# Performance work log

Hardware: AMD Instinct MI355X
Metric: run time of the kernel (lower is better)

## Reference

```python
import jax, jax.numpy as jnp
import numpy as np

NH = 8
DIM = 512
NP = 1024
MNP = 4096
BS = 4
TOPK = 32


def setup_inputs() -> dict:
    key = jax.random.key(0)
    ks = jax.random.split(key, 10)
    q = jax.random.normal(ks[0], (NP, BS, DIM), dtype=jnp.float32)
    k = jax.random.normal(ks[1], (MNP, BS, DIM), dtype=jnp.float32)
    v = jax.random.normal(ks[2], (MNP, BS, DIM), dtype=jnp.float32)
    rns_indices = jax.random.randint(ks[3], (BS, NP, TOPK), 0, MNP)
    s = 0.02
    W1 = jax.random.normal(ks[4], (DIM, DIM), dtype=jnp.float32) * s
    b1 = jnp.zeros((DIM,), dtype=jnp.float32)
    W2 = jax.random.normal(ks[5], (DIM, DIM), dtype=jnp.float32) * s
    b2 = jnp.zeros((DIM,), dtype=jnp.float32)
    W3 = jax.random.normal(ks[6], (DIM, DIM), dtype=jnp.float32) * s
    b3 = jnp.zeros((DIM,), dtype=jnp.float32)
    return {"q": q, "k": k, "v": v, "rns_indices": rns_indices,
            "W1": W1, "b1": b1, "W2": W2, "b2": b2, "W3": W3, "b3": b3}


def reference(q, k, v, rns_indices, W1, b1, W2, b2, W3, b3):
    np_, bs, dim = q.shape
    mnp = k.shape[0]
    nh = NH
    dh = dim // nh
    # seq-first -> batch-first, linear projections (torch Linear: x @ W.T + b)
    qh = (jnp.einsum('nbd,ed->bne', q, W1) + b1).reshape(bs, np_, nh, dh)
    kh = (jnp.einsum('mbd,ed->bme', k, W2) + b2).reshape(bs, mnp, nh, dh)
    vh = (jnp.einsum('mbd,ed->bme', v, W3) + b3).reshape(bs, mnp, nh, dh)
    # dense scores: [bs, nh, np, mnp]
    w = jnp.einsum('bnhd,bmhd->bhnm', qh, kh) / jnp.sqrt(jnp.asarray(dh, w_dtype := qh.dtype))
    # scatter-built neighbor mask: [bs, np, mnp] (shared across heads)
    b_idx = jnp.arange(bs)[:, None, None]
    n_idx = jnp.arange(np_)[None, :, None]
    mask = jnp.zeros((bs, np_, mnp), dtype=w.dtype).at[b_idx, n_idx, rns_indices].set(1.0)
    mask = mask[:, None, :, :]  # broadcast over heads
    w = w * mask + (-1e9) * (1.0 - mask)
    w = jax.nn.softmax(w, axis=3)
    out = jnp.einsum('bhnm,bmhd->nbhd', w, vh).reshape(np_, bs, dim)
    return out
```

## Files before the change

kernel.cpp:

```cpp
#include <hip/hip_runtime.h>
#include <stdint.h>

#define NH   8
#define DIM  512
#define NP   1024
#define MNP  4096
#define BS   4
#define TOPK 32
#define DH   64

typedef unsigned short u16;
typedef __attribute__((ext_vector_type(8))) short bf16x8;
typedef __attribute__((ext_vector_type(4))) float f32x4;

__device__ __forceinline__ u16 f2bf(float f) {
    union { float f; unsigned u; } x; x.f = f;
    unsigned r = x.u + 0x7FFFu + ((x.u >> 16) & 1u);
    return (u16)(r >> 16);
}
__device__ __forceinline__ float bf2f(u16 h) {
    union { unsigned u; float f; } x; x.u = ((unsigned)h) << 16;
    return x.f;
}

__device__ __forceinline__ void async16(const void* g, void* l) {
    __builtin_amdgcn_global_load_lds(
        (const __attribute__((address_space(1))) unsigned int*)g,
        (__attribute__((address_space(3))) unsigned int*)l, 16, 0, 0);
}

__global__ void cvt_all(const float* __restrict__ W1, const float* __restrict__ W2,
                        const float* __restrict__ W3, const float* __restrict__ q,
                        const float* __restrict__ k,  const float* __restrict__ v,
                        u16* __restrict__ wall, u16* __restrict__ act) {
    size_t i = ((size_t)blockIdx.x * 256 + threadIdx.x) * 4;
    const float* s; u16* d;
    if (i < 786432) {
        d = wall + i;
        s = (i < 262144) ? W1 + i : (i < 524288) ? W2 + (i - 262144) : W3 + (i - 524288);
    } else {
        size_t j = i - 786432;
        d = act + j;
        s = (j < 2097152) ? q + j : (j < 10485760) ? k + (j - 2097152) : v + (j - 10485760);
    }
    float4 val = *(const float4*)s;
    ushort4 o;
    o.x = f2bf(val.x); o.y = f2bf(val.y); o.z = f2bf(val.z); o.w = f2bf(val.w);
    *(ushort4*)d = o;
}

__global__ __launch_bounds__(256, 2)
void proj_gemm(const u16* __restrict__ act, const u16* __restrict__ wall,
               const float* __restrict__ b1, const float* __restrict__ b2,
               const float* __restrict__ b3, u16* __restrict__ outall) {
    __shared__ u16 As[128 * 64];
    __shared__ u16 Bs[128 * 64];

    const int z = blockIdx.z;
    if (z == 0 && blockIdx.y >= 32) return;
    const size_t aoff = (z == 0) ? 0u : (z == 1) ? 2097152u : 10485760u;
    const u16* A = act + aoff;
    const u16* W = wall + (size_t)z * 262144;
    const float* bias = (z == 0) ? b1 : (z == 1) ? b2 : b3;
    u16* C = outall + aoff;

    const int tid  = threadIdx.x;
    const int bm   = blockIdx.y * 128;
    const int bn   = blockIdx.x * 128;
    const int wave = tid >> 6;
    const int lane = tid & 63;
    const int wm   = (wave & 1) * 64;
    const int wn   = (wave >> 1) * 64;
    const int l16  = lane & 15;
    const int quad = lane >> 4;

    const int srow = lane >> 3;
    const int scol = (lane & 7) * 8;

    f32x4 acc[4][4] = {};

    for (int k0 = 0; k0 < 512; k0 += 64) {
        __syncthreads();
#pragma unroll
        for (int r = 0; r < 4; r++) {
            int row = wave * 32 + r * 8;
            async16(A + (size_t)(bm + row + srow) * 512 + k0 + scol,
                    &As[row * 64 + lane * 8]);
            async16(W + (size_t)(bn + row + srow) * 512 + k0 + scol,
                    &Bs[row * 64 + lane * 8]);
        }
        __syncthreads();
#pragma unroll
        for (int kk = 0; kk < 64; kk += 32) {
            bf16x8 af[4], bfr[4];
#pragma unroll
            for (int i = 0; i < 4; i++) {
                af[i]  = *(const bf16x8*)(&As[(wm + i * 16 + l16) * 64 + kk + quad * 8]);
                bfr[i] = *(const bf16x8*)(&Bs[(wn + i * 16 + l16) * 64 + kk + quad * 8]);
            }
#pragma unroll
            for (int i = 0; i < 4; i++)
#pragma unroll
                for (int j = 0; j < 4; j++)
                    acc[i][j] = __builtin_amdgcn_mfma_f32_16x16x32_bf16(
                        af[i], bfr[j], acc[i][j], 0, 0, 0);
        }
    }
#pragma unroll
    for (int i = 0; i < 4; i++) {
        int row = bm + wm + i * 16 + quad * 4;
#pragma unroll
        for (int j = 0; j < 4; j++) {
            int col = bn + wn + j * 16 + l16;
            float bv = bias[col];
#pragma unroll
            for (int r = 0; r < 4; r++)
                C[(size_t)(row + r) * 512 + col] = f2bf(acc[i][j][r] + bv);
        }
    }
}

__global__ __launch_bounds__(256)
void attn_kernel(const u16* __restrict__ Qh, const u16* __restrict__ Kh,
                 const u16* __restrict__ Vh, const int* __restrict__ rns,
                 float* __restrict__ out) {
    __shared__ float sq[NH * 72];
    __shared__ int   sidx[TOPK];
    __shared__ int   srow[TOPK];
    __shared__ float sval[TOPK];
    __shared__ float ss[TOPK][9];
    __shared__ float sw[TOPK][9];

    const int bid = blockIdx.x;
    const int n = bid >> 2;
    const int b = bid & 3;
    const int tid = threadIdx.x;
    const int lane = tid & 63;

    if (tid < TOPK) {
        int mi = rns[((b * NP + n) * TOPK) + tid];
        sidx[tid] = mi;
        srow[tid] = (mi * BS + b) * DIM;
    }
    {
        const u16* qrow = Qh + (size_t)(n * BS + b) * DIM;
        unsigned int u = *(const unsigned int*)(qrow + tid * 2);
        int e0 = tid * 2;
        sq[(e0 >> 6) * 72 + (e0 & 63)]       = bf2f((u16)(u & 0xffff));
        sq[(e0 >> 6) * 72 + ((e0 + 1) & 63)] = bf2f((u16)(u >> 16));
    }
    __syncthreads();
    if (tid < TOPK) {
        float v = 1.0f;
        int me = sidx[tid];
        for (int j = 0; j < tid; j++)
            if (sidx[j] == me) v = 0.0f;
        sval[tid] = v;
    }
    __syncthreads();
    {
        const int i = tid >> 3;
        const int h = tid & 7;
        const u16* krow = Kh + srow[i] + h * DH;
        const float* qh = sq + h * 72;
        float acc = 0.f;
#pragma unroll
        for (int d = 0; d < DH; d += 8) {
            uint4 kv = *(const uint4*)(krow + d);
            float4 qa = *(const float4*)(qh + d);
            float4 qb = *(const float4*)(qh + d + 4);
            acc += qa.x * bf2f((u16)(kv.x & 0xffff)) + qa.y * bf2f((u16)(kv.x >> 16))
                 + qa.z * bf2f((u16)(kv.y & 0xffff)) + qa.w * bf2f((u16)(kv.y >> 16))
                 + qb.x * bf2f((u16)(kv.z & 0xffff)) + qb.y * bf2f((u16)(kv.z >> 16))
                 + qb.z * bf2f((u16)(kv.w & 0xffff)) + qb.w * bf2f((u16)(kv.w >> 16));
        }
        ss[i][h] = (sval[i] > 0.f) ? acc * 0.125f : -1e30f;
    }
    __syncthreads();
    {
        const int h = tid >> 5;
        const int i = tid & 31;
        float val = ss[i][h];
        float m = val;
#pragma unroll
        for (int msk = 1; msk < 32; msk <<= 1) m = fmaxf(m, __shfl_xor(m, msk, 64));
        float e = __expf(val - m);
        float s = e;
#pragma unroll
        for (int msk = 1; msk < 32; msk <<= 1) s += __shfl_xor(s, msk, 64);
        sw[i][h] = e / s;
    }
    __syncthreads();
    {
        const int wv   = tid >> 6;
        const int part = lane & 3;
        const int e8   = (wv * 16 + (lane >> 2)) * 8;
        const int h    = e8 >> 6;
        float a[8] = {0, 0, 0, 0, 0, 0, 0, 0};
#pragma unroll
        for (int j = 0; j < 8; j++) {
            int i = part * 8 + j;
            float w = sw[i][h];
            uint4 vv = *(const uint4*)(Vh + srow[i] + e8);
            a[0] += w * bf2f((u16)(vv.x & 0xffff)); a[1] += w * bf2f((u16)(vv.x >> 16));
            a[2] += w * bf2f((u16)(vv.y & 0xffff)); a[3] += w * bf2f((u16)(vv.y >> 16));
            a[4] += w * bf2f((u16)(vv.z & 0xffff)); a[5] += w * bf2f((u16)(vv.z >> 16));
            a[6] += w * bf2f((u16)(vv.w & 0xffff)); a[7] += w * bf2f((u16)(vv.w >> 16));
        }
#pragma unroll
        for (int j = 0; j < 8; j++) {
            a[j] += __shfl_xor(a[j], 1, 64);
            a[j] += __shfl_xor(a[j], 2, 64);
        }
        if (part == 0) {
            float* op = out + (size_t)(n * BS + b) * DIM + e8;
            float4 o0 = {a[0], a[1], a[2], a[3]};
            float4 o1 = {a[4], a[5], a[6], a[7]};
            *(float4*)op = o0;
            *((float4*)op + 1) = o1;
        }
    }
}

extern "C" void kernel_launch(void* const* d_in, const int* in_sizes, int n_in,
                              void* d_out, int out_size, void* d_ws, size_t ws_size,
                              hipStream_t stream) {
    const float* q  = (const float*)d_in[0];
    const float* k  = (const float*)d_in[1];
    const float* v  = (const float*)d_in[2];
    const int* rns  = (const int*)d_in[3];
    const float* W1 = (const float*)d_in[4];
    const float* b1 = (const float*)d_in[5];
    const float* W2 = (const float*)d_in[6];
    const float* b2 = (const float*)d_in[7];
    const float* W3 = (const float*)d_in[8];
    const float* b3 = (const float*)d_in[9];
    float* out = (float*)d_out;

    u16* ws   = (u16*)d_ws;
    u16* wall = ws;
    u16* act  = wall + 786432;
    u16* proj = act + 18874368;
    u16* Qh = proj;
    u16* Kh = proj + 2097152;
    u16* Vh = proj + 10485760;

    cvt_all<<<19200, 256, 0, stream>>>(W1, W2, W3, q, k, v, wall, act);
    proj_gemm<<<dim3(4, 128, 3), 256, 0, stream>>>(act, wall, b1, b2, b3, proj);
    attn_kernel<<<NP * BS, 256, 0, stream>>>(Qh, Kh, Vh, rns, out);
}
```

Baseline: 198.7 us.

## Assign one wavefront per query-batch pair in sparse attention kernel

```diff
diff --git a/kernel.cpp b/kernel.cpp
--- a/kernel.cpp
+++ b/kernel.cpp
@@ -124,102 +124,105 @@
 void attn_kernel(const u16* __restrict__ Qh, const u16* __restrict__ Kh,
                  const u16* __restrict__ Vh, const int* __restrict__ rns,
                  float* __restrict__ out) {
-    __shared__ float sq[NH * 72];
-    __shared__ int   sidx[TOPK];
-    __shared__ int   srow[TOPK];
-    __shared__ float sval[TOPK];
-    __shared__ float ss[TOPK][9];
-    __shared__ float sw[TOPK][9];
-
-    const int bid = blockIdx.x;
-    const int n = bid >> 2;
-    const int b = bid & 3;
-    const int tid = threadIdx.x;
-    const int lane = tid & 63;
-
-    if (tid < TOPK) {
-        int mi = rns[((b * NP + n) * TOPK) + tid];
-        sidx[tid] = mi;
-        srow[tid] = (mi * BS + b) * DIM;
-    }
+    __shared__ float sq[4][512];
+    __shared__ float swt[4][32 * 9];
+    __shared__ int   srw[4][TOPK];
+
+    const int wv   = threadIdx.x >> 6;
+    const int lane = threadIdx.x & 63;
+    const int pair = blockIdx.x * 4 + wv;
+    const int n = pair >> 2;
+    const int b = pair & 3;
+    const int s   = lane >> 1;
+    const int sub = lane & 1;
+
+    int myidx = rns[(b * NP + n) * TOPK + s];
+    int myrow = (myidx * BS + b) * DIM;
+    if (sub == 0) srw[wv][s] = myrow;
+
+    bool dup = false;
+#pragma unroll
+    for (int j = 0; j < TOPK; j++) {
+        int other = __shfl(myidx, j * 2, 64);
+        dup = dup || ((j < s) && (other == myidx));
+    }
+
     {
-        const u16* qrow = Qh + (size_t)(n * BS + b) * DIM;
-        unsigned int u = *(const unsigned int*)(qrow + tid * 2);
-        int e0 = tid * 2;
-        sq[(e0 >> 6) * 72 + (e0 & 63)]       = bf2f((u16)(u & 0xffff));
-        sq[(e0 >> 6) * 72 + ((e0 + 1) & 63)] = bf2f((u16)(u >> 16));
-    }
-    __syncthreads();
-    if (tid < TOPK) {
-        float v = 1.0f;
-        int me = sidx[tid];
-        for (int j = 0; j < tid; j++)
-            if (sidx[j] == me) v = 0.0f;
-        sval[tid] = v;
-    }
-    __syncthreads();
-    {
-        const int i = tid >> 3;
-        const int h = tid & 7;
-        const u16* krow = Kh + srow[i] + h * DH;
-        const float* qh = sq + h * 72;
+        const u16* qrow = Qh + (size_t)pair * DIM;
+        uint4 qv = *(const uint4*)(qrow + lane * 8);
+        float4 f0 = { bf2f((u16)qv.x), bf2f((u16)(qv.x >> 16)),
+                      bf2f((u16)qv.y), bf2f((u16)(qv.y >> 16)) };
+        float4 f1 = { bf2f((u16)qv.z), bf2f((u16)(qv.z >> 16)),
+                      bf2f((u16)qv.w), bf2f((u16)(qv.w >> 16)) };
+        *(float4*)(&sq[wv][lane * 8])     = f0;
+        *(float4*)(&sq[wv][lane * 8 + 4]) = f1;
+    }
+    __builtin_amdgcn_wave_barrier();
+
+    const float* qw = sq[wv];
+    float sc[NH];
+#pragma unroll
+    for (int h = 0; h < NH; h++) {
+        const u16* kp = Kh + myrow + h * DH + sub * 32;
+        const float* qp = qw + h * DH + sub * 32;
         float acc = 0.f;
 #pragma unroll
-        for (int d = 0; d < DH; d += 8) {
-            uint4 kv = *(const uint4*)(krow + d);
-            float4 qa = *(const float4*)(qh + d);
-            float4 qb = *(const float4*)(qh + d + 4);
-            acc += qa.x * bf2f((u16)(kv.x & 0xffff)) + qa.y * bf2f((u16)(kv.x >> 16))
-                 + qa.z * bf2f((u16)(kv.y & 0xffff)) + qa.w * bf2f((u16)(kv.y >> 16))
-                 + qb.x * bf2f((u16)(kv.z & 0xffff)) + qb.y * bf2f((u16)(kv.z >> 16))
-                 + qb.z * bf2f((u16)(kv.w & 0xffff)) + qb.w * bf2f((u16)(kv.w >> 16));
-        }
-        ss[i][h] = (sval[i] > 0.f) ? acc * 0.125f : -1e30f;
-    }
-    __syncthreads();
-    {
-        const int h = tid >> 5;
-        const int i = tid & 31;
-        float val = ss[i][h];
-        float m = val;
-#pragma unroll
-        for (int msk = 1; msk < 32; msk <<= 1) m = fmaxf(m, __shfl_xor(m, msk, 64));
-        float e = __expf(val - m);
-        float s = e;
-#pragma unroll
-        for (int msk = 1; msk < 32; msk <<= 1) s += __shfl_xor(s, msk, 64);
-        sw[i][h] = e / s;
-    }
-    __syncthreads();
-    {
-        const int wv   = tid >> 6;
-        const int part = lane & 3;
-        const int e8   = (wv * 16 + (lane >> 2)) * 8;
-        const int h    = e8 >> 6;
-        float a[8] = {0, 0, 0, 0, 0, 0, 0, 0};
-#pragma unroll
-        for (int j = 0; j < 8; j++) {
-            int i = part * 8 + j;
-            float w = sw[i][h];
-            uint4 vv = *(const uint4*)(Vh + srow[i] + e8);
-            a[0] += w * bf2f((u16)(vv.x & 0xffff)); a[1] += w * bf2f((u16)(vv.x >> 16));
-            a[2] += w * bf2f((u16)(vv.y & 0xffff)); a[3] += w * bf2f((u16)(vv.y >> 16));
-            a[4] += w * bf2f((u16)(vv.z & 0xffff)); a[5] += w * bf2f((u16)(vv.z >> 16));
-            a[6] += w * bf2f((u16)(vv.w & 0xffff)); a[7] += w * bf2f((u16)(vv.w >> 16));
-        }
-#pragma unroll
-        for (int j = 0; j < 8; j++) {
-            a[j] += __shfl_xor(a[j], 1, 64);
-            a[j] += __shfl_xor(a[j], 2, 64);
-        }
-        if (part == 0) {
-            float* op = out + (size_t)(n * BS + b) * DIM + e8;
-            float4 o0 = {a[0], a[1], a[2], a[3]};
-            float4 o1 = {a[4], a[5], a[6], a[7]};
-            *(float4*)op = o0;
-            *((float4*)op + 1) = o1;
-        }
-    }
+        for (int d = 0; d < 32; d += 8) {
+            uint4 kv = *(const uint4*)(kp + d);
+            acc += qp[d + 0] * bf2f((u16)kv.x) + qp[d + 1] * bf2f((u16)(kv.x >> 16))
+                 + qp[d + 2] * bf2f((u16)kv.y) + qp[d + 3] * bf2f((u16)(kv.y >> 16))
+                 + qp[d + 4] * bf2f((u16)kv.z) + qp[d + 5] * bf2f((u16)(kv.z >> 16))
+                 + qp[d + 6] * bf2f((u16)kv.w) + qp[d + 7] * bf2f((u16)(kv.w >> 16));
+        }
+        sc[h] = acc;
+    }
+#pragma unroll
+    for (int h = 0; h < NH; h++) {
+        sc[h] += __shfl_xor(sc[h], 1, 64);
+        sc[h] = dup ? -1e30f : sc[h] * 0.125f;
+    }
+    float w[NH];
+#pragma unroll
+    for (int h = 0; h < NH; h++) {
+        float m = sc[h];
+        m = fmaxf(m, __shfl_xor(m, 2, 64));
+        m = fmaxf(m, __shfl_xor(m, 4, 64));
+        m = fmaxf(m, __shfl_xor(m, 8, 64));
+        m = fmaxf(m, __shfl_xor(m, 16, 64));
+        m = fmaxf(m, __shfl_xor(m, 32, 64));
+        float e = __expf(sc[h] - m);
+        float t = e;
+        t += __shfl_xor(t, 2, 64);
+        t += __shfl_xor(t, 4, 64);
+        t += __shfl_xor(t, 8, 64);
+        t += __shfl_xor(t, 16, 64);
+        t += __shfl_xor(t, 32, 64);
+        w[h] = e / t;
+    }
+    if (sub == 0) {
+#pragma unroll
+        for (int h = 0; h < NH; h++) swt[wv][s * 9 + h] = w[h];
+    }
+    __builtin_amdgcn_wave_barrier();
+
+    const int h  = lane >> 3;
+    const int e8 = lane * 8;
+    float a[8] = {0, 0, 0, 0, 0, 0, 0, 0};
+#pragma unroll 8
+    for (int si = 0; si < TOPK; si++) {
+        int   row = srw[wv][si];
+        float wgt = swt[wv][si * 9 + h];
+        uint4 vv = *(const uint4*)(Vh + row + e8);
+        a[0] += wgt * bf2f((u16)vv.x); a[1] += wgt * bf2f((u16)(vv.x >> 16));
+        a[2] += wgt * bf2f((u16)vv.y); a[3] += wgt * bf2f((u16)(vv.y >> 16));
+        a[4] += wgt * bf2f((u16)vv.z); a[5] += wgt * bf2f((u16)(vv.z >> 16));
+        a[6] += wgt * bf2f((u16)vv.w); a[7] += wgt * bf2f((u16)(vv.w >> 16));
+    }
+    float* op = out + (size_t)pair * DIM + e8;
+    float4 o0 = {a[0], a[1], a[2], a[3]};
+    float4 o1 = {a[4], a[5], a[6], a[7]};
+    *(float4*)op       = o0;
+    *((float4*)op + 1) = o1;
 }
 
 extern "C" void kernel_launch(void* const* d_in, const int* in_sizes, int n_in,
@@ -247,5 +250,5 @@
 
     cvt_all<<<19200, 256, 0, stream>>>(W1, W2, W3, q, k, v, wall, act);
     proj_gemm<<<dim3(4, 128, 3), 256, 0, stream>>>(act, wall, b1, b2, b3, proj);
-    attn_kernel<<<NP * BS, 256, 0, stream>>>(Qh, Kh, Vh, rns, out);
-}
+    attn_kernel<<<NP * BS / 4, 256, 0, stream>>>(Qh, Kh, Vh, rns, out);
+}
```

Result: faster. 189.2 us (-4.8%).
